# Optimization experiments

Measured on AMD Instinct MI355X. Metric: run time of the kernel, lower is better.

## Reference

```python
import math
import jax, jax.numpy as jnp
import numpy as np

H = 16  # head_count

def setup_inputs() -> dict:
    key = jax.random.key(0)
    ks = jax.random.split(key, 7)
    B, S, D = 2, 2048, 1024
    query = jax.random.normal(ks[0], (B, S, D), dtype=jnp.float32)
    # mask: True = masked position (matches masked_fill_ semantics)
    mask = jax.random.randint(ks[1], (B, S, S), 0, 2) > 0
    scale = 1.0 / math.sqrt(D)  # xavier-ish init scale
    Wq = jax.random.normal(ks[2], (D, D), dtype=jnp.float32) * scale
    Wk = jax.random.normal(ks[3], (D, D), dtype=jnp.float32) * scale
    Wv = jax.random.normal(ks[4], (D, D), dtype=jnp.float32) * scale
    Wo = jax.random.normal(ks[5], (D, D), dtype=jnp.float32) * scale
    bo = jnp.zeros((D,), dtype=jnp.float32)
    return {"query": query, "mask": mask, "Wq": Wq, "Wk": Wk, "Wv": Wv, "Wo": Wo, "bo": bo}


def reference(query, mask, Wq, Wk, Wv, Wo, bo):
    B, S, D = query.shape
    dh = D // H

    def split_heads(x):  # [B,S,D] -> [B,H,S,dh]
        return x.reshape(B, S, H, dh).transpose(0, 2, 1, 3)

    # torch nn.Linear computes x @ W.T (bias-free for q/k/v)
    q = split_heads(query @ Wq.T) * (1.0 / math.sqrt(dh))
    k = split_heads(query @ Wk.T)
    v = split_heads(query @ Wv.T)

    scores = jnp.einsum('bhqd,bhkd->bhqk', q, k)           # [B,H,S,S]
    scores = jnp.where(mask[:, None, :, :], jnp.float32(-1e18), scores)
    weights = jax.nn.softmax(scores, axis=-1)               # dropout=0 -> identity
    ctx = jnp.einsum('bhqk,bhkd->bhqd', weights, v)         # [B,H,S,dh]
    ctx = ctx.transpose(0, 2, 1, 3).reshape(B, S, D)        # combine heads
    return ctx @ Wo.T + bo
```

## Files before the change

### kernel.cpp

```cpp
#include <hip/hip_runtime.h>

#define S_LEN 2048
#define D_MODEL 1024
#define NH 16
#define DH 64

typedef __bf16 bf16x8 __attribute__((ext_vector_type(8)));
typedef __bf16 bf16x4 __attribute__((ext_vector_type(4)));
typedef float f32x4 __attribute__((ext_vector_type(4)));

__device__ __forceinline__ unsigned short f2bf(float f) {
  unsigned int x = __float_as_uint(f);
  x += 0x7fffu + ((x >> 16) & 1u);
  return (unsigned short)(x >> 16);
}

__device__ __forceinline__ bf16x4 cvt4(f32x4 v) {
  return __builtin_convertvector(v, bf16x4);
}

__device__ __forceinline__ float exp2raw(float x) {
#if __has_builtin(__builtin_amdgcn_exp2f)
  return __builtin_amdgcn_exp2f(x);
#else
  return exp2f(x);
#endif
}

__device__ __forceinline__ f32x4 mfma16(bf16x8 a, bf16x8 b, f32x4 c) {
  return __builtin_amdgcn_mfma_f32_16x16x32_bf16(a, b, c, 0, 0, 0);
}

__device__ __forceinline__ void gl2lds(const unsigned short* g, unsigned short* l) {
  __builtin_amdgcn_global_load_lds(
      (__attribute__((address_space(1))) void*)g,
      (__attribute__((address_space(3))) void*)l, 16, 0, 0);
}

__global__ __launch_bounds__(256) void prep_kernel(
    const float* __restrict__ q, const float* __restrict__ wq,
    const float* __restrict__ wk, const float* __restrict__ wv,
    const float* __restrict__ wo, const int* __restrict__ mask,
    unsigned short* __restrict__ qbf, unsigned short* __restrict__ wbf,
    unsigned long long* __restrict__ bits) {
  const int bx = blockIdx.x;
  if (bx < 32768) {
    int i = bx * 256 + threadIdx.x;
    unsigned long long bal = __ballot(mask[i] != 0);
    if ((threadIdx.x & 63) == 0) bits[i >> 6] = bal;
  } else {
    const long t = (long)(bx - 32768) * 256 + threadIdx.x;
    const float* src;
    unsigned short* dst;
    long e;
    if (t < 524288) { src = q; dst = qbf; e = t * 8; }
    else {
      long u = t - 524288;
      int wi = (int)(u >> 17);
      e = (u & 131071) * 8;
      src = wi == 0 ? wq : wi == 1 ? wk : wi == 2 ? wv : wo;
      dst = wbf + (long)wi * 1048576;
    }
    float4 a = *(const float4*)(src + e);
    float4 b = *(const float4*)(src + e + 4);
    ushort4 p0 = {f2bf(a.x), f2bf(a.y), f2bf(a.z), f2bf(a.w)};
    ushort4 p1 = {f2bf(b.x), f2bf(b.y), f2bf(b.z), f2bf(b.w)};
    *(ushort4*)(dst + e) = p0;
    *(ushort4*)(dst + e + 4) = p1;
  }
}

__global__ __launch_bounds__(256) void gemm_qkv(
    const unsigned short* __restrict__ A, const unsigned short* __restrict__ W3,
    unsigned short* __restrict__ qb, unsigned short* __restrict__ kb,
    unsigned short* __restrict__ vt, float qscale) {
  __shared__ unsigned short As[128 * 64];
  __shared__ unsigned short Bs[128 * 64];
  const int tid = threadIdx.x, lane = tid & 63, wid = tid >> 6;
  const int wm = wid >> 1, wn = wid & 1;
  const int quad = lane >> 4, c = lane & 15, cx = c & 7;
  const int nG = blockIdx.x * 128;
  const int wi = nG >> 10, nn0 = nG & 1023;
  const int m0 = blockIdx.y * 128;
  const unsigned short* Bsrc = W3 + (size_t)wi * 1048576;
  const int srow = lane >> 3;
  const int schk = ((lane & 7) ^ srow) * 8;
  const unsigned short* ag = A + (size_t)(m0 + wid * 32 + srow) * 1024 + schk;
  const unsigned short* bg = Bsrc + (size_t)(nn0 + wid * 32 + srow) * 1024 + schk;
  f32x4 acc[4][4] = {};
  for (int kk = 0; kk < 1024; kk += 64) {
#pragma unroll
    for (int i = 0; i < 4; ++i) {
      gl2lds(ag + (size_t)(i * 8) * 1024 + kk, &As[(wid * 32 + i * 8) * 64]);
      gl2lds(bg + (size_t)(i * 8) * 1024 + kk, &Bs[(wid * 32 + i * 8) * 64]);
    }
    __syncthreads();
#pragma unroll
    for (int kc = 0; kc < 2; ++kc) {
      bf16x8 a[4], b[4];
#pragma unroll
      for (int mt = 0; mt < 4; ++mt)
        a[mt] = *(const bf16x8*)(
            &As[(wm * 64 + mt * 16 + c) * 64 + ((kc * 4 + quad) ^ cx) * 8]);
#pragma unroll
      for (int nt = 0; nt < 4; ++nt)
        b[nt] = *(const bf16x8*)(
            &Bs[(wn * 64 + nt * 16 + c) * 64 + ((kc * 4 + quad) ^ cx) * 8]);
#pragma unroll
      for (int mt = 0; mt < 4; ++mt)
#pragma unroll
        for (int nt = 0; nt < 4; ++nt)
          acc[mt][nt] = mfma16(a[mt], b[nt], acc[mt][nt]);
    }
    __syncthreads();
  }
#pragma unroll
  for (int mt = 0; mt < 4; ++mt) {
#pragma unroll
    for (int nt = 0; nt < 4; ++nt) {
      const int mb = m0 + wm * 64 + mt * 16 + quad * 4;
      const int n = nn0 + wn * 64 + nt * 16 + c;
      const int hh = n >> 6, d = n & 63;
      const int bb = mb >> 11, ss = mb & 2047;
      if (wi == 0) {
#pragma unroll
        for (int r = 0; r < 4; ++r)
          qb[(size_t)((bb * NH + hh) * S_LEN + ss + r) * DH + d] =
              f2bf(acc[mt][nt][r] * qscale);
      } else if (wi == 1) {
#pragma unroll
        for (int r = 0; r < 4; ++r)
          kb[(size_t)((bb * NH + hh) * S_LEN + ss + r) * DH + d] =
              f2bf(acc[mt][nt][r]);
      } else {
        *(bf16x4*)(vt + (size_t)((bb * NH + hh) * DH + d) * S_LEN + ss) =
            cvt4(acc[mt][nt]);
      }
    }
  }
}

__global__ __launch_bounds__(256) void gemm_out(
    const unsigned short* __restrict__ A, const unsigned short* __restrict__ W,
    float* __restrict__ out, const float* __restrict__ bias) {
  __shared__ unsigned short As[128 * 128];
  __shared__ unsigned short Bs[64 * 128];
  const int tid = threadIdx.x, lane = tid & 63, wid = tid >> 6;
  const int wm = wid >> 1, wn = wid & 1;
  const int quad = lane >> 4, c = lane & 15, cx = c & 7;
  const int n0 = blockIdx.x * 64, m0 = blockIdx.y * 128;
  const int srow4 = lane >> 4, sch = lane & 15;
  const int co0 = (sch ^ srow4) * 8;
  const int co1 = (sch ^ (4 + srow4)) * 8;
  const unsigned short* agr = A + (size_t)(m0 + wid * 32 + srow4) * 1024;
  const unsigned short* bgr = W + (size_t)(n0 + wid * 16 + srow4) * 1024;
  f32x4 acc[4][2] = {};
  for (int kk = 0; kk < 1024; kk += 128) {
#pragma unroll
    for (int i = 0; i < 8; ++i)
      gl2lds(agr + (size_t)(i * 4) * 1024 + kk + ((i & 1) ? co1 : co0),
             &As[(wid * 32 + i * 4) * 128]);
#pragma unroll
    for (int i = 0; i < 4; ++i)
      gl2lds(bgr + (size_t)(i * 4) * 1024 + kk + ((i & 1) ? co1 : co0),
             &Bs[(wid * 16 + i * 4) * 128]);
    __syncthreads();
#pragma unroll
    for (int kc = 0; kc < 4; ++kc) {
      bf16x8 a[4], b[2];
#pragma unroll
      for (int mt = 0; mt < 4; ++mt)
        a[mt] = *(const bf16x8*)(
            &As[(wm * 64 + mt * 16 + c) * 128 + ((kc * 4 + quad) ^ cx) * 8]);
#pragma unroll
      for (int nt = 0; nt < 2; ++nt)
        b[nt] = *(const bf16x8*)(
            &Bs[(wn * 32 + nt * 16 + c) * 128 + ((kc * 4 + quad) ^ cx) * 8]);
#pragma unroll
      for (int mt = 0; mt < 4; ++mt)
#pragma unroll
        for (int nt = 0; nt < 2; ++nt)
          acc[mt][nt] = mfma16(a[mt], b[nt], acc[mt][nt]);
    }
    __syncthreads();
  }
#pragma unroll
  for (int mt = 0; mt < 4; ++mt) {
#pragma unroll
    for (int nt = 0; nt < 2; ++nt) {
      const int mb = m0 + wm * 64 + mt * 16 + quad * 4;
      const int n = n0 + wn * 32 + nt * 16 + c;
      const float bv = bias[n];
#pragma unroll
      for (int r = 0; r < 4; ++r)
        out[(size_t)(mb + r) * D_MODEL + n] = acc[mt][nt][r] + bv;
    }
  }
}

__global__ __launch_bounds__(256, 2) void attn_kernel(
    const unsigned short* __restrict__ qb, const unsigned short* __restrict__ kb,
    const unsigned short* __restrict__ vt,
    const unsigned long long* __restrict__ mbits,
    unsigned short* __restrict__ ctx) {
  const int h = blockIdx.x, qt = blockIdx.y, b = blockIdx.z;
  const int bh = b * NH + h;
  const int tid = threadIdx.x, lane = tid & 63, wid = tid >> 6;
  const int quad = lane >> 4, c = lane & 15, cx = c & 7;
  const int qw = wid & 1, kh = wid >> 1;
  const int q0 = qt * 128;
  __shared__ __align__(16) char smem[65536];
  unsigned short* KVb = (unsigned short*)smem;

  const int qbase = q0 + qw * 64;
  const unsigned short* qp = qb + (size_t)(bh * S_LEN + qbase + c) * DH;
  bf16x8 bq[4][2];
#pragma unroll
  for (int sub = 0; sub < 4; ++sub) {
    bq[sub][0] = *(const bf16x8*)(qp + sub * 16 * DH + quad * 8);
    bq[sub][1] = *(const bf16x8*)(qp + sub * 16 * DH + 32 + quad * 8);
  }

  const bf16x8 onesv = {(__bf16)1.f, (__bf16)1.f, (__bf16)1.f, (__bf16)1.f,
                        (__bf16)1.f, (__bf16)1.f, (__bf16)1.f, (__bf16)1.f};

  f32x4 o[4][4] = {};
  float lacc[4] = {0.f, 0.f, 0.f, 0.f};
  const unsigned long long* mq0 =
      mbits + (size_t)(b * S_LEN + qbase + c) * 32 + kh * 16;

  const int srow = lane >> 3, schk = ((lane & 7) ^ srow) * 8;

  const unsigned short* gKb =
      kb + (size_t)(bh * S_LEN + (wid & 1) * 1024) * DH + schk;
  const unsigned short* gV =
      vt + (size_t)(bh * DH + srow) * S_LEN + (wid - 2) * 1024 + schk;

  for (int kt = 0; kt < 1024; kt += 128) {
    if (wid < 2) {
#pragma unroll
      for (int hf = 0; hf < 2; ++hf)
#pragma unroll
        for (int i = 0; i < 8; ++i) {
          const int t = i * 8 + srow;
          const int st = (t & 0x23) | ((t >> 2) & 0x04) | ((t << 1) & 0x18);
          gl2lds(gKb + (size_t)(kt + hf * 64 + st) * DH,
                 &KVb[hf * 16384 + wid * 4096 + i * 512]);
        }
    } else {
#pragma unroll
      for (int hf = 0; hf < 2; ++hf)
#pragma unroll
        for (int i = 0; i < 8; ++i)
          gl2lds(gV + (size_t)(i * 8) * S_LEN + kt + hf * 64,
                 &KVb[hf * 16384 + wid * 4096 + i * 512]);
    }
    __syncthreads();

#pragma unroll
    for (int hf = 0; hf < 2; ++hf) {
      const unsigned short* Ksh = KVb + hf * 16384 + kh * 4096;
      const unsigned short* Vsh = KVb + hf * 16384 + (2 + kh) * 4096;
      const int mi = (kt >> 6) + hf;

      bf16x8 kf[8];
#pragma unroll
      for (int g = 0; g < 4; ++g) {
        const int rho = g * 16 + c;
        kf[2 * g] = *(const bf16x8*)(&Ksh[rho * 64 + (quad ^ cx) * 8]);
        kf[2 * g + 1] =
            *(const bf16x8*)(&Ksh[rho * 64 + ((4 + quad) ^ cx) * 8]);
      }

      bf16x8 bps[4][2];
#pragma unroll
      for (int sub = 0; sub < 4; ++sub) {
        f32x4 s[4];
        __builtin_amdgcn_s_setprio(1);
#pragma unroll
        for (int g = 0; g < 4; ++g) {
          f32x4 z = {};
          z = mfma16(kf[2 * g], bq[sub][0], z);
          z = mfma16(kf[2 * g + 1], bq[sub][1], z);
          s[g] = z;
        }
        __builtin_amdgcn_s_setprio(0);
        const unsigned long long w64 = mq0[sub * 512 + mi];
        const unsigned int wlo = (unsigned int)w64;
        const unsigned int whi = (unsigned int)(w64 >> 32);
        f32x4 p[4];
#pragma unroll
        for (int g = 0; g < 4; ++g) {
          const unsigned int bits =
              ((g & 2) ? whi : wlo) >> (quad * 8 + (g & 1) * 4);
#pragma unroll
          for (int r = 0; r < 4; ++r) {
            const float e = exp2raw(s[g][r]);
            p[g][r] = ((bits >> r) & 1u) ? 0.f : e;
          }
        }
        union { bf16x8 v; bf16x4 h[2]; } u0, u1;
        u0.h[0] = cvt4(p[0]); u0.h[1] = cvt4(p[1]);
        u1.h[0] = cvt4(p[2]); u1.h[1] = cvt4(p[3]);
        bps[sub][0] = u0.v;
        bps[sub][1] = u1.v;
        f32x4 zs = {};
        zs = mfma16(onesv, bps[sub][0], zs);
        zs = mfma16(onesv, bps[sub][1], zs);
        lacc[sub] += zs[0];
      }

      __builtin_amdgcn_s_setprio(1);
#pragma unroll
      for (int ks = 0; ks < 2; ++ks) {
#pragma unroll
        for (int nt = 0; nt < 4; ++nt) {
          bf16x8 av = *(const bf16x8*)(
              &Vsh[(nt * 16 + c) * 64 + ((ks * 4 + quad) ^ cx) * 8]);
#pragma unroll
          for (int sub = 0; sub < 4; ++sub)
            o[sub][nt] = mfma16(av, bps[sub][ks], o[sub][nt]);
        }
      }
      __builtin_amdgcn_s_setprio(0);
    }
    __syncthreads();
  }

  float* mrg = (float*)smem;
  float* ml = mrg + 8 * 1088;
  if (kh == 1) {
#pragma unroll
    for (int sub = 0; sub < 4; ++sub) {
      float* mo = mrg + (qw * 4 + sub) * 1088;
#pragma unroll
      for (int nt = 0; nt < 4; ++nt)
        *(f32x4*)(mo + c * 68 + nt * 16 + quad * 4) = o[sub][nt];
      if (quad == 0) ml[(qw * 4 + sub) * 16 + c] = lacc[sub];
    }
  }
  __syncthreads();
  if (kh == 0) {
#pragma unroll
    for (int sub = 0; sub < 4; ++sub) {
      const int pp = qw * 4 + sub;
      const float inv = 1.0f / (lacc[sub] + ml[pp * 16 + c]);
      const int q = qbase + sub * 16 + c;
      const float* mo = mrg + pp * 1088;
#pragma unroll
      for (int nt = 0; nt < 4; ++nt) {
        f32x4 ob = *(const f32x4*)(mo + c * 68 + nt * 16 + quad * 4);
        f32x4 rr = (o[sub][nt] + ob) * inv;
        *(bf16x4*)(ctx + (size_t)(b * S_LEN + q) * D_MODEL + h * DH + nt * 16 +
                   quad * 4) = cvt4(rr);
      }
    }
  }
}

extern "C" void kernel_launch(void* const* d_in, const int* in_sizes, int n_in,
                              void* d_out, int out_size, void* d_ws, size_t ws_size,
                              hipStream_t stream) {
  const float* query = (const float*)d_in[0];
  const int* mask = (const int*)d_in[1];
  const float* Wq = (const float*)d_in[2];
  const float* Wk = (const float*)d_in[3];
  const float* Wv = (const float*)d_in[4];
  const float* Wo = (const float*)d_in[5];
  const float* bo = (const float*)d_in[6];
  float* out = (float*)d_out;

  char* ws = (char*)d_ws;
  const size_t MB = 1024 * 1024;
  unsigned short* qbf = (unsigned short*)(ws);
  unsigned short* wbf = (unsigned short*)(ws + 8 * MB);
  unsigned short* qb = (unsigned short*)(ws + 16 * MB);
  unsigned short* kb = (unsigned short*)(ws + 24 * MB);
  unsigned short* vt = (unsigned short*)(ws + 32 * MB);
  unsigned long long* mb = (unsigned long long*)(ws + 40 * MB);
  unsigned short* ctx = qbf;

  prep_kernel<<<32768 + 4096, 256, 0, stream>>>(query, Wq, Wk, Wv, Wo, mask,
                                                qbf, wbf, mb);

  gemm_qkv<<<dim3(3072 / 128, 4096 / 128), 256, 0, stream>>>(
      qbf, wbf, qb, kb, vt, 0.18033688f);

  attn_kernel<<<dim3(NH, S_LEN / 128, 2), 256, 0, stream>>>(qb, kb, vt, mb,
                                                            ctx);

  gemm_out<<<dim3(1024 / 64, 4096 / 128), 256, 0, stream>>>(
      ctx, wbf + 3 * 1048576, out, bo);
}
```

Baseline: 219.2 us.

## Double-buffer K/V LDS tiles and prefetch mask words one step ahead

The attention loop now loads 64-key K/V tiles into two alternating LDS buffers. The next tile's global-to-LDS copy is issued before computing on the current one, with a partial vmcnt wait so the copy overlaps the MFMA work. Mask bit words are also prefetched into registers one iteration ahead. This aims to hide global memory latency that the old load-then-sync-then-compute loop exposed, at the cost of smaller per-iteration tiles and more barriers. It also relies on hand-written waitcnt counts being correct, including the mask loads that are counted in vmcnt.

```diff
diff --git a/kernel.cpp b/kernel.cpp
--- a/kernel.cpp
+++ b/kernel.cpp
@@ -236,96 +236,108 @@
   const unsigned short* gV =
       vt + (size_t)(bh * DH + srow) * S_LEN + (wid - 2) * 1024 + schk;
 
-  for (int kt = 0; kt < 1024; kt += 128) {
-    if (wid < 2) {
-#pragma unroll
-      for (int hf = 0; hf < 2; ++hf)
-#pragma unroll
-        for (int i = 0; i < 8; ++i) {
-          const int t = i * 8 + srow;
-          const int st = (t & 0x23) | ((t >> 2) & 0x04) | ((t << 1) & 0x18);
-          gl2lds(gKb + (size_t)(kt + hf * 64 + st) * DH,
-                 &KVb[hf * 16384 + wid * 4096 + i * 512]);
-        }
+#define STAGE(buf, kt)                                                        \
+  do {                                                                        \
+    unsigned short* dst = KVb + (buf)*16384 + wid * 4096;                     \
+    if (wid < 2) {                                                            \
+      _Pragma("unroll") for (int i = 0; i < 8; ++i) {                         \
+        const int t2 = i * 8 + srow;                                          \
+        const int st =                                                        \
+            (t2 & 0x23) | ((t2 >> 2) & 0x04) | ((t2 << 1) & 0x18);            \
+        gl2lds(gKb + (size_t)((kt) + st) * DH, &dst[i * 512]);                \
+      }                                                                       \
+    } else {                                                                  \
+      _Pragma("unroll") for (int i = 0; i < 8; ++i)                           \
+          gl2lds(gV + (size_t)(i * 8) * S_LEN + (kt), &dst[i * 512]);         \
+    }                                                                         \
+  } while (0)
+
+  unsigned long long wmc[4];
+#pragma unroll
+  for (int sub = 0; sub < 4; ++sub) wmc[sub] = mq0[sub * 512];
+  STAGE(0, 0);
+
+  for (int t = 0; t < 16; ++t) {
+    const int cur = t & 1;
+    unsigned long long wmn[4];
+    if (t < 15) {
+      STAGE(cur ^ 1, (t + 1) * 64);
+#pragma unroll
+      for (int sub = 0; sub < 4; ++sub) wmn[sub] = mq0[sub * 512 + t + 1];
+      asm volatile("s_waitcnt vmcnt(12)" ::: "memory");
     } else {
-#pragma unroll
-      for (int hf = 0; hf < 2; ++hf)
-#pragma unroll
-        for (int i = 0; i < 8; ++i)
-          gl2lds(gV + (size_t)(i * 8) * S_LEN + kt + hf * 64,
-                 &KVb[hf * 16384 + wid * 4096 + i * 512]);
-    }
-    __syncthreads();
-
-#pragma unroll
-    for (int hf = 0; hf < 2; ++hf) {
-      const unsigned short* Ksh = KVb + hf * 16384 + kh * 4096;
-      const unsigned short* Vsh = KVb + hf * 16384 + (2 + kh) * 4096;
-      const int mi = (kt >> 6) + hf;
-
-      bf16x8 kf[8];
+      asm volatile("s_waitcnt vmcnt(0)" ::: "memory");
+    }
+    __builtin_amdgcn_s_barrier();
+
+    const unsigned short* Ksh = KVb + cur * 16384 + kh * 4096;
+    const unsigned short* Vsh = KVb + cur * 16384 + (2 + kh) * 4096;
+
+    bf16x8 kf[8];
+#pragma unroll
+    for (int g = 0; g < 4; ++g) {
+      const int rho = g * 16 + c;
+      kf[2 * g] = *(const bf16x8*)(&Ksh[rho * 64 + (quad ^ cx) * 8]);
+      kf[2 * g + 1] = *(const bf16x8*)(&Ksh[rho * 64 + ((4 + quad) ^ cx) * 8]);
+    }
+
+    bf16x8 bps[4][2];
+#pragma unroll
+    for (int sub = 0; sub < 4; ++sub) {
+      f32x4 s[4];
+      __builtin_amdgcn_s_setprio(1);
 #pragma unroll
       for (int g = 0; g < 4; ++g) {
-        const int rho = g * 16 + c;
-        kf[2 * g] = *(const bf16x8*)(&Ksh[rho * 64 + (quad ^ cx) * 8]);
-        kf[2 * g + 1] =
-            *(const bf16x8*)(&Ksh[rho * 64 + ((4 + quad) ^ cx) * 8]);
+        f32x4 z = {};
+        z = mfma16(kf[2 * g], bq[sub][0], z);
+        z = mfma16(kf[2 * g + 1], bq[sub][1], z);
+        s[g] = z;
       }
-
-      bf16x8 bps[4][2];
-#pragma unroll
-      for (int sub = 0; sub < 4; ++sub) {
-        f32x4 s[4];
-        __builtin_amdgcn_s_setprio(1);
-#pragma unroll
-        for (int g = 0; g < 4; ++g) {
-          f32x4 z = {};
-          z = mfma16(kf[2 * g], bq[sub][0], z);
-          z = mfma16(kf[2 * g + 1], bq[sub][1], z);
-          s[g] = z;
-        }
-        __builtin_amdgcn_s_setprio(0);
-        const unsigned long long w64 = mq0[sub * 512 + mi];
-        const unsigned int wlo = (unsigned int)w64;
-        const unsigned int whi = (unsigned int)(w64 >> 32);
-        f32x4 p[4];
-#pragma unroll
-        for (int g = 0; g < 4; ++g) {
-          const unsigned int bits =
-              ((g & 2) ? whi : wlo) >> (quad * 8 + (g & 1) * 4);
-#pragma unroll
-          for (int r = 0; r < 4; ++r) {
-            const float e = exp2raw(s[g][r]);
-            p[g][r] = ((bits >> r) & 1u) ? 0.f : e;
-          }
-        }
-        union { bf16x8 v; bf16x4 h[2]; } u0, u1;
-        u0.h[0] = cvt4(p[0]); u0.h[1] = cvt4(p[1]);
-        u1.h[0] = cvt4(p[2]); u1.h[1] = cvt4(p[3]);
-        bps[sub][0] = u0.v;
-        bps[sub][1] = u1.v;
-        f32x4 zs = {};
-        zs = mfma16(onesv, bps[sub][0], zs);
-        zs = mfma16(onesv, bps[sub][1], zs);
-        lacc[sub] += zs[0];
-      }
-
-      __builtin_amdgcn_s_setprio(1);
-#pragma unroll
-      for (int ks = 0; ks < 2; ++ks) {
-#pragma unroll
-        for (int nt = 0; nt < 4; ++nt) {
-          bf16x8 av = *(const bf16x8*)(
-              &Vsh[(nt * 16 + c) * 64 + ((ks * 4 + quad) ^ cx) * 8]);
-#pragma unroll
-          for (int sub = 0; sub < 4; ++sub)
-            o[sub][nt] = mfma16(av, bps[sub][ks], o[sub][nt]);
+      __builtin_amdgcn_s_setprio(0);
+      const unsigned long long w64 = wmc[sub];
+      const unsigned int wlo = (unsigned int)w64;
+      const unsigned int whi = (unsigned int)(w64 >> 32);
+      f32x4 p[4];
+#pragma unroll
+      for (int g = 0; g < 4; ++g) {
+        const unsigned int bits =
+            ((g & 2) ? whi : wlo) >> (quad * 8 + (g & 1) * 4);
+#pragma unroll
+        for (int r = 0; r < 4; ++r) {
+          const float e = exp2raw(s[g][r]);
+          p[g][r] = ((bits >> r) & 1u) ? 0.f : e;
         }
       }
-      __builtin_amdgcn_s_setprio(0);
-    }
-    __syncthreads();
-  }
+      union { bf16x8 v; bf16x4 h[2]; } u0, u1;
+      u0.h[0] = cvt4(p[0]); u0.h[1] = cvt4(p[1]);
+      u1.h[0] = cvt4(p[2]); u1.h[1] = cvt4(p[3]);
+      bps[sub][0] = u0.v;
+      bps[sub][1] = u1.v;
+      f32x4 zs = {};
+      zs = mfma16(onesv, bps[sub][0], zs);
+      zs = mfma16(onesv, bps[sub][1], zs);
+      lacc[sub] += zs[0];
+    }
+
+    __builtin_amdgcn_s_setprio(1);
+#pragma unroll
+    for (int ks = 0; ks < 2; ++ks) {
+#pragma unroll
+      for (int nt = 0; nt < 4; ++nt) {
+        bf16x8 av = *(const bf16x8*)(
+            &Vsh[(nt * 16 + c) * 64 + ((ks * 4 + quad) ^ cx) * 8]);
+#pragma unroll
+        for (int sub = 0; sub < 4; ++sub)
+          o[sub][nt] = mfma16(av, bps[sub][ks], o[sub][nt]);
+      }
+    }
+    __builtin_amdgcn_s_setprio(0);
+
+#pragma unroll
+    for (int sub = 0; sub < 4; ++sub) wmc[sub] = wmn[sub];
+    __builtin_amdgcn_s_barrier();
+  }
+#undef STAGE
 
   float* mrg = (float*)smem;
   float* ml = mrg + 8 * 1088;
```

After: 224.8 us. 1.03x slower.

## Fold mask bit-packing into QKV GEMM grid to overlap with matmul

Applied to the files above, without the earlier changes.

Mask ballot-packing moves out of the prep kernel and into extra blocks of the QKV GEMM launch. The GEMM grid grows to 24x374, and only every 12th y-row does GEMM work. The memory-bound mask read can then run alongside the compute-bound projection GEMM instead of before it. Each mask block now packs 16 words with 4 ballots per wave. The cost is more complex block indexing and some scheduling interference with the GEMM tiles.

```diff
diff --git a/kernel.cpp b/kernel.cpp
--- a/kernel.cpp
+++ b/kernel.cpp
@@ -8,6 +8,8 @@
 typedef __bf16 bf16x8 __attribute__((ext_vector_type(8)));
 typedef __bf16 bf16x4 __attribute__((ext_vector_type(4)));
 typedef float f32x4 __attribute__((ext_vector_type(4)));
+typedef unsigned short us8 __attribute__((ext_vector_type(8)));
+typedef unsigned long long ull2 __attribute__((ext_vector_type(2)));
 
 __device__ __forceinline__ unsigned short f2bf(float f) {
   unsigned int x = __float_as_uint(f);
@@ -40,40 +42,51 @@
 __global__ __launch_bounds__(256) void prep_kernel(
     const float* __restrict__ q, const float* __restrict__ wq,
     const float* __restrict__ wk, const float* __restrict__ wv,
-    const float* __restrict__ wo, const int* __restrict__ mask,
-    unsigned short* __restrict__ qbf, unsigned short* __restrict__ wbf,
-    unsigned long long* __restrict__ bits) {
-  const int bx = blockIdx.x;
-  if (bx < 32768) {
-    int i = bx * 256 + threadIdx.x;
-    unsigned long long bal = __ballot(mask[i] != 0);
-    if ((threadIdx.x & 63) == 0) bits[i >> 6] = bal;
-  } else {
-    const long t = (long)(bx - 32768) * 256 + threadIdx.x;
-    const float* src;
-    unsigned short* dst;
-    long e;
-    if (t < 524288) { src = q; dst = qbf; e = t * 8; }
-    else {
-      long u = t - 524288;
-      int wi = (int)(u >> 17);
-      e = (u & 131071) * 8;
-      src = wi == 0 ? wq : wi == 1 ? wk : wi == 2 ? wv : wo;
-      dst = wbf + (long)wi * 1048576;
-    }
-    float4 a = *(const float4*)(src + e);
-    float4 b = *(const float4*)(src + e + 4);
-    ushort4 p0 = {f2bf(a.x), f2bf(a.y), f2bf(a.z), f2bf(a.w)};
-    ushort4 p1 = {f2bf(b.x), f2bf(b.y), f2bf(b.z), f2bf(b.w)};
-    *(ushort4*)(dst + e) = p0;
-    *(ushort4*)(dst + e + 4) = p1;
-  }
+    const float* __restrict__ wo, unsigned short* __restrict__ qbf,
+    unsigned short* __restrict__ wbf) {
+  const long t = (long)blockIdx.x * 256 + threadIdx.x;
+  const float* src;
+  unsigned short* dst;
+  long e;
+  if (t < 524288) { src = q; dst = qbf; e = t * 8; }
+  else {
+    long u = t - 524288;
+    int wi = (int)(u >> 17);
+    e = (u & 131071) * 8;
+    src = wi == 0 ? wq : wi == 1 ? wk : wi == 2 ? wv : wo;
+    dst = wbf + (long)wi * 1048576;
+  }
+  float4 a = *(const float4*)(src + e);
+  float4 b = *(const float4*)(src + e + 4);
+  ushort4 p0 = {f2bf(a.x), f2bf(a.y), f2bf(a.z), f2bf(a.w)};
+  ushort4 p1 = {f2bf(b.x), f2bf(b.y), f2bf(b.z), f2bf(b.w)};
+  *(ushort4*)(dst + e) = p0;
+  *(ushort4*)(dst + e + 4) = p1;
 }
 
 __global__ __launch_bounds__(256) void gemm_qkv(
     const unsigned short* __restrict__ A, const unsigned short* __restrict__ W3,
     unsigned short* __restrict__ qb, unsigned short* __restrict__ kb,
-    unsigned short* __restrict__ vt, float qscale) {
+    unsigned short* __restrict__ vt, const int* __restrict__ mask,
+    unsigned long long* __restrict__ bits, float qscale) {
+  if (blockIdx.y % 12 != 0) {
+    const int mi = blockIdx.y - blockIdx.y / 12 - 1;
+    const int mblk = mi * 24 + blockIdx.x;
+    if (mblk < 8192) {
+      const int wv = threadIdx.x >> 6, ln = threadIdx.x & 63;
+      const long wbase = (long)mblk * 16 + wv * 4;
+      unsigned long long w[4];
+#pragma unroll
+      for (int j = 0; j < 4; ++j)
+        w[j] = __ballot(mask[(wbase + j) * 64 + ln] != 0);
+      if (ln == 0) {
+        ull2 lo = {w[0], w[1]}, hi = {w[2], w[3]};
+        *(ull2*)(bits + wbase) = lo;
+        *(ull2*)(bits + wbase + 2) = hi;
+      }
+    }
+    return;
+  }
   __shared__ unsigned short As[128 * 64];
   __shared__ unsigned short Bs[128 * 64];
   const int tid = threadIdx.x, lane = tid & 63, wid = tid >> 6;
@@ -81,7 +94,7 @@
   const int quad = lane >> 4, c = lane & 15, cx = c & 7;
   const int nG = blockIdx.x * 128;
   const int wi = nG >> 10, nn0 = nG & 1023;
-  const int m0 = blockIdx.y * 128;
+  const int m0 = (blockIdx.y / 12) * 128;
   const unsigned short* Bsrc = W3 + (size_t)wi * 1048576;
   const int srow = lane >> 3;
   const int schk = ((lane & 7) ^ srow) * 8;
@@ -380,11 +393,10 @@
   unsigned long long* mb = (unsigned long long*)(ws + 40 * MB);
   unsigned short* ctx = qbf;
 
-  prep_kernel<<<32768 + 4096, 256, 0, stream>>>(query, Wq, Wk, Wv, Wo, mask,
-                                                qbf, wbf, mb);
-
-  gemm_qkv<<<dim3(3072 / 128, 4096 / 128), 256, 0, stream>>>(
-      qbf, wbf, qb, kb, vt, 0.18033688f);
+  prep_kernel<<<4096, 256, 0, stream>>>(query, Wq, Wk, Wv, Wo, qbf, wbf);
+
+  gemm_qkv<<<dim3(24, 374), 256, 0, stream>>>(qbf, wbf, qb, kb, vt, mask, mb,
+                                              0.18033688f);
 
   attn_kernel<<<dim3(NH, S_LEN / 128, 2), 256, 0, stream>>>(qb, kb, vt, mb,
                                                             ctx);
```

Measured after the change: 231.0 us. +5.4%, slower.
